# Optimization experiments

Hardware: AMD Instinct MI355X
Metric: run time of the kernel (lower is better)

## Reference

```python
import jax, jax.numpy as jnp
import numpy as np

V, FC = 6890, 13776
N, H, W, K = 2, 336, 336, 28
SIGMA, GAMMA, EPS = 1e-4, 1e-4, 1e-10
ZNEAR, ZFAR = 1.0, 100.0
SHININESS = 64.0
BG = jnp.array([1.0, 1.0, 1.0], jnp.float32)


def setup_inputs() -> dict:
    key = jax.random.key(0)
    ks = jax.random.split(key, 10)
    verts = jax.random.normal(ks[0], (V, 3), jnp.float32)
    vert_colors = jax.random.uniform(ks[1], (V, 3), jnp.float32)
    faces = jax.random.randint(ks[2], (FC, 3), 0, V)
    # shift so ~1/FC entries are -1 (background), as in PyTorch3D Fragments
    pix_to_face = jax.random.randint(ks[3], (N, H, W, K), 0, FC + 1) - 1
    u = jax.random.uniform(ks[4], (N, H, W, K, 3), jnp.float32) + 1e-3
    bary_coords = u / u.sum(-1, keepdims=True)
    dists = jax.random.normal(ks[5], (N, H, W, K), jnp.float32) * 1e-4
    zbuf = jnp.sort(jax.random.uniform(ks[6], (N, H, W, K), jnp.float32) * 10.0 + 2.0, axis=-1)
    light_location = jnp.array([0.0, 0.0, 10.0], jnp.float32)
    ambient_color = jnp.full((3,), 0.5, jnp.float32)
    diffuse_color = jnp.full((3,), 0.3, jnp.float32)
    specular_color = jnp.full((3,), 0.2, jnp.float32)
    camera_position = jnp.array([0.0, 0.0, 2.7], jnp.float32)
    return dict(verts=verts, vert_colors=vert_colors, faces=faces,
                pix_to_face=pix_to_face, bary_coords=bary_coords, dists=dists,
                zbuf=zbuf, light_location=light_location,
                ambient_color=ambient_color, diffuse_color=diffuse_color,
                specular_color=specular_color, camera_position=camera_position)


def _normalize(x, eps=1e-6):
    return x / jnp.maximum(jnp.linalg.norm(x, axis=-1, keepdims=True), eps)


def reference(verts, vert_colors, faces, pix_to_face, bary_coords, dists, zbuf,
              light_location, ambient_color, diffuse_color, specular_color,
              camera_position):
    # ---- per-vertex normals (area-weighted face normals scatter-added) ----
    v0, v1, v2 = verts[faces[:, 0]], verts[faces[:, 1]], verts[faces[:, 2]]
    fn = jnp.cross(v1 - v0, v2 - v0)                       # [F,3]
    fn_rep = jnp.repeat(fn[:, None, :], 3, axis=1).reshape(-1, 3)
    vnorm = jax.ops.segment_sum(fn_rep, faces.reshape(-1), num_segments=verts.shape[0])
    vnorm = _normalize(vnorm)                              # [V,3]

    # ---- gather face attributes per fragment & barycentric interpolation ----
    mask = pix_to_face >= 0                                # [N,H,W,K]
    idx = jnp.maximum(pix_to_face, 0)
    f = faces[idx]                                         # [N,H,W,K,3]
    pix_pos = jnp.einsum('nhwkc,nhwkcd->nhwkd', bary_coords, verts[f])
    pix_nrm = _normalize(jnp.einsum('nhwkc,nhwkcd->nhwkd', bary_coords, vnorm[f]))
    texels = jnp.einsum('nhwkc,nhwkcd->nhwkd', bary_coords, vert_colors[f])

    # ---- Phong shading (point light) ----
    l = _normalize(light_location - pix_pos)               # [N,H,W,K,3]
    ndotl = jnp.maximum(jnp.sum(pix_nrm * l, axis=-1), 0.0)
    diffuse = diffuse_color * ndotl[..., None]
    view = _normalize(camera_position - pix_pos)
    reflect = -l + 2.0 * jnp.sum(l * pix_nrm, axis=-1, keepdims=True) * pix_nrm
    cos_a = jnp.maximum(jnp.sum(reflect * view, axis=-1), 0.0)
    specular = specular_color * (cos_a ** SHININESS)[..., None]
    colors = (ambient_color + diffuse) * texels + specular  # [N,H,W,K,3]

    # ---- softmax_rgb_blend ----
    prob = jax.nn.sigmoid(-dists / SIGMA) * mask            # [N,H,W,K]
    z_inv = jnp.where(mask, (ZFAR - zbuf) / (ZFAR - ZNEAR), 0.0)
    z_inv_max = jnp.maximum(z_inv.max(axis=-1, keepdims=True), EPS)
    w_num = prob * jnp.exp((z_inv - z_inv_max) / GAMMA)     # [N,H,W,K]
    delta = jnp.exp((EPS - z_inv_max) / GAMMA)              # [N,H,W,1]
    denom = w_num.sum(axis=-1, keepdims=True) + delta       # [N,H,W,1]
    rgb = (jnp.einsum('nhwk,nhwkd->nhwd', w_num, colors) + delta * BG) / denom
    alpha = 1.0 - jnp.prod(1.0 - prob, axis=-1)             # [N,H,W]
    images = jnp.concatenate([rgb, alpha[..., None]], axis=-1)  # [N,H,W,4]
    return images, zbuf
```

## Files before the change

kernel.cpp:

```cpp
#include <hip/hip_runtime.h>
#include <hip/hip_fp16.h>
#include <math.h>

#define V_   6890
#define FC_  13776
#define N_   2
#define H_   336
#define W_   336
#define K_   28
#define NPIX (N_*H_*W_)

#define SIGMA_INV 1.0e4f
#define GAMMA_INV 1.0e4f
#define EPS_      1e-10f
#define ZFAR_     100.0f
#define ZSCALE    (1.0f/99.0f)
#define LOG2E     1.442695041f
#define SKIP_EXPONENT 25.0f

typedef float f32x4 __attribute__((ext_vector_type(4)));

static __device__ __forceinline__ float fexp(float x)  { return __builtin_amdgcn_exp2f(x * LOG2E); }
static __device__ __forceinline__ float frcp(float x)  { return __builtin_amdgcn_rcpf(x); }
static __device__ __forceinline__ float frsq(float x)  { return __builtin_amdgcn_rsqf(x); }

#define FD_OFFSET 82944

union FaceRec { uint4 q[4]; float f[16]; __half h[32]; unsigned char b[64]; };

__global__ __launch_bounds__(256)
void face_normals(const float* __restrict__ verts,
                  const int*   __restrict__ faces,
                  float* __restrict__ vnAcc) {
    int i = blockIdx.x * blockDim.x + threadIdx.x;
    if (i >= FC_) return;
    int f0 = faces[i*3+0], f1 = faces[i*3+1], f2 = faces[i*3+2];
    float p0x = verts[f0*3+0], p0y = verts[f0*3+1], p0z = verts[f0*3+2];
    float p1x = verts[f1*3+0], p1y = verts[f1*3+1], p1z = verts[f1*3+2];
    float p2x = verts[f2*3+0], p2y = verts[f2*3+1], p2z = verts[f2*3+2];
    float e1x = p1x-p0x, e1y = p1y-p0y, e1z = p1z-p0z;
    float e2x = p2x-p0x, e2y = p2y-p0y, e2z = p2z-p0z;
    float fnx = e1y*e2z - e1z*e2y;
    float fny = e1z*e2x - e1x*e2z;
    float fnz = e1x*e2y - e1y*e2x;
    atomicAdd(&vnAcc[f0*3+0], fnx); atomicAdd(&vnAcc[f0*3+1], fny); atomicAdd(&vnAcc[f0*3+2], fnz);
    atomicAdd(&vnAcc[f1*3+0], fnx); atomicAdd(&vnAcc[f1*3+1], fny); atomicAdd(&vnAcc[f1*3+2], fnz);
    atomicAdd(&vnAcc[f2*3+0], fnx); atomicAdd(&vnAcc[f2*3+1], fny); atomicAdd(&vnAcc[f2*3+2], fnz);
}

__global__ __launch_bounds__(256)
void face_pack(const int*   __restrict__ faces,
               const float* __restrict__ verts,
               const float* __restrict__ vcol,
               const float* __restrict__ vn,
               uint4* __restrict__ fd) {
    int i = blockIdx.x * blockDim.x + threadIdx.x;
    if (i >= FC_) return;
    FaceRec R;
    #pragma unroll
    for (int v = 0; v < 3; ++v) {
        int fv = faces[i*3+v];
        R.f[v*3+0] = verts[fv*3+0];
        R.f[v*3+1] = verts[fv*3+1];
        R.f[v*3+2] = verts[fv*3+2];
        float nx = vn[fv*3+0], ny = vn[fv*3+1], nz = vn[fv*3+2];
        float inv = frsq(fmaxf(nx*nx + ny*ny + nz*nz, 1e-12f));
        R.h[18+v*3+0] = __float2half(nx*inv);
        R.h[18+v*3+1] = __float2half(ny*inv);
        R.h[18+v*3+2] = __float2half(nz*inv);
        R.b[54+v*3+0] = (unsigned char)lrintf(vcol[fv*3+0]*255.0f);
        R.b[54+v*3+1] = (unsigned char)lrintf(vcol[fv*3+1]*255.0f);
        R.b[54+v*3+2] = (unsigned char)lrintf(vcol[fv*3+2]*255.0f);
    }
    R.b[63] = 0;
    uint4* o = fd + (size_t)i * 4;
    o[0] = R.q[0]; o[1] = R.q[1]; o[2] = R.q[2]; o[3] = R.q[3];
}

__global__ __launch_bounds__(256)
void pixel_kernel(const int*   __restrict__ ptf,
                  const float* __restrict__ bary,
                  const float* __restrict__ dists,
                  const float* __restrict__ zbuf,
                  const uint4* __restrict__ fd,
                  const float* __restrict__ light,
                  const float* __restrict__ amb,
                  const float* __restrict__ dif,
                  const float* __restrict__ spec,
                  const float* __restrict__ cam,
                  float* __restrict__ out) {
    int tid = blockIdx.x * blockDim.x + threadIdx.x;
    int pix = tid >> 3;
    int j   = tid & 7;

    float lx = light[0], ly = light[1], lz = light[2];
    float cx = cam[0],   cy = cam[1],   cz = cam[2];
    float a0 = amb[0],  a1 = amb[1],  a2 = amb[2];
    float f0 = dif[0],  f1 = dif[1],  f2 = dif[2];
    float s0 = spec[0], s1 = spec[1], s2 = spec[2];

    float wsum = 0.0f, sr = 0.0f, sg = 0.0f, sb = 0.0f;
    float om = 1.0f;
    float mloc = 0.0f;

    int   pfs[4]  = {-1,-1,-1,-1};
    float zi[4]   = {0,0,0,0};
    float prob[4] = {0,0,0,0};
    bool lane_act = (j < 7);
    size_t sbase = (size_t)pix * K_ + (size_t)j * 4;

    if (lane_act) {
        int4   pf4 = *(const int4*)  (ptf   + sbase);
        float4 d4  = *(const float4*)(dists + sbase);
        float4 z4  = *(const float4*)(zbuf  + sbase);

        f32x4 znt = { z4.x, z4.y, z4.z, z4.w };
        __builtin_nontemporal_store(znt, (f32x4*)(out + (size_t)NPIX*4 + sbase));

        pfs[0]=pf4.x; pfs[1]=pf4.y; pfs[2]=pf4.z; pfs[3]=pf4.w;
        float ds_[4] = {d4.x, d4.y, d4.z, d4.w};
        float zs_[4] = {z4.x, z4.y, z4.z, z4.w};

        #pragma unroll
        for (int s = 0; s < 4; ++s) {
            zi[s] = (ZFAR_ - zs_[s]) * ZSCALE;
            bool a = (pfs[s] >= 0);
            float pr = frcp(1.0f + fexp(ds_[s] * SIGMA_INV));
            prob[s] = a ? pr : 0.0f;
            if (a) mloc = fmaxf(mloc, zi[s]);
            om *= (1.0f - prob[s]);
        }
    }

    float m = mloc;
    m = fmaxf(m, __shfl_xor(m, 1));
    m = fmaxf(m, __shfl_xor(m, 2));
    m = fmaxf(m, __shfl_xor(m, 4));
    m = fmaxf(m, EPS_);

    #pragma unroll
    for (int s = 0; s < 4; ++s) {
        float ex = (zi[s] - m) * GAMMA_INV;
        bool keep = (pfs[s] >= 0) && (ex >= -SKIP_EXPONENT);
        if (keep) {
            size_t smp = sbase + (size_t)s;
            float3 bv = *(const float3*)(bary + smp*3);
            float w0 = bv.x, w1 = bv.y, w2 = bv.z;

            FaceRec F;
            const uint4* g = fd + (size_t)pfs[s] * 4;
            F.q[0] = g[0]; F.q[1] = g[1]; F.q[2] = g[2]; F.q[3] = g[3];

            float px = w0*F.f[0] + w1*F.f[3] + w2*F.f[6];
            float py = w0*F.f[1] + w1*F.f[4] + w2*F.f[7];
            float pz = w0*F.f[2] + w1*F.f[5] + w2*F.f[8];
            float nux = w0*__half2float(F.h[18]) + w1*__half2float(F.h[21]) + w2*__half2float(F.h[24]);
            float nuy = w0*__half2float(F.h[19]) + w1*__half2float(F.h[22]) + w2*__half2float(F.h[25]);
            float nuz = w0*__half2float(F.h[20]) + w1*__half2float(F.h[23]) + w2*__half2float(F.h[26]);
            const float s255 = 1.0f/255.0f;
            float tr = (w0*(float)F.b[54] + w1*(float)F.b[57] + w2*(float)F.b[60]) * s255;
            float tg = (w0*(float)F.b[55] + w1*(float)F.b[58] + w2*(float)F.b[61]) * s255;
            float tb = (w0*(float)F.b[56] + w1*(float)F.b[59] + w2*(float)F.b[62]) * s255;

            float ninv = frsq(fmaxf(nux*nux + nuy*nuy + nuz*nuz, 1e-12f));
            float nx = nux*ninv, ny = nuy*ninv, nz = nuz*ninv;

            float lvx = lx - px, lvy = ly - py, lvz = lz - pz;
            float linv = frsq(fmaxf(lvx*lvx + lvy*lvy + lvz*lvz, 1e-12f));
            lvx *= linv; lvy *= linv; lvz *= linv;
            float ldn = lvx*nx + lvy*ny + lvz*nz;
            float ndotl = fmaxf(ldn, 0.0f);

            float vvx = cx - px, vvy = cy - py, vvz = cz - pz;
            float vinv = frsq(fmaxf(vvx*vvx + vvy*vvy + vvz*vvz, 1e-12f));
            vvx *= vinv; vvy *= vinv; vvz *= vinv;

            float rx = 2.0f*ldn*nx - lvx;
            float ry = 2.0f*ldn*ny - lvy;
            float rz = 2.0f*ldn*nz - lvz;
            float ca = fmaxf(rx*vvx + ry*vvy + rz*vvz, 0.0f);
            float p64 = ca*ca; p64 *= p64; p64 *= p64; p64 *= p64; p64 *= p64; p64 *= p64;

            float cr = (a0 + f0*ndotl)*tr + s0*p64;
            float cg = (a1 + f1*ndotl)*tg + s1*p64;
            float cb = (a2 + f2*ndotl)*tb + s2*p64;

            float w = prob[s] * fexp(ex);
            wsum += w; sr += w*cr; sg += w*cg; sb += w*cb;
        }
    }

    #pragma unroll
    for (int o = 4; o; o >>= 1) {
        wsum += __shfl_xor(wsum, o);
        sr   += __shfl_xor(sr,   o);
        sg   += __shfl_xor(sg,   o);
        sb   += __shfl_xor(sb,   o);
        om   *= __shfl_xor(om,   o);
    }

    if (j == 0) {
        float deltaw = fexp((EPS_ - m) * GAMMA_INV);
        float inv = frcp(wsum + deltaw);
        float4 img;
        img.x = (sr + deltaw) * inv;
        img.y = (sg + deltaw) * inv;
        img.z = (sb + deltaw) * inv;
        img.w = 1.0f - om;
        ((float4*)out)[pix] = img;
    }
}

extern "C" void kernel_launch(void* const* d_in, const int* in_sizes, int n_in,
                              void* d_out, int out_size, void* d_ws, size_t ws_size,
                              hipStream_t stream) {
    const float* verts = (const float*)d_in[0];
    const float* vcol  = (const float*)d_in[1];
    const int*   faces = (const int*)d_in[2];
    const int*   ptf   = (const int*)d_in[3];
    const float* bary  = (const float*)d_in[4];
    const float* dists = (const float*)d_in[5];
    const float* zbuf  = (const float*)d_in[6];
    const float* light = (const float*)d_in[7];
    const float* amb   = (const float*)d_in[8];
    const float* dif   = (const float*)d_in[9];
    const float* spec  = (const float*)d_in[10];
    const float* cam   = (const float*)d_in[11];
    float* out = (float*)d_out;

    float* vnAcc = (float*)d_ws;
    uint4* fdat  = (uint4*)((char*)d_ws + FD_OFFSET);

    (void)hipMemsetAsync(vnAcc, 0, (size_t)V_ * 3 * sizeof(float), stream);
    face_normals<<<(FC_ + 255)/256, 256, 0, stream>>>(verts, faces, vnAcc);
    face_pack<<<(FC_ + 255)/256, 256, 0, stream>>>(faces, verts, vcol, vnAcc, fdat);

    int blocks = (NPIX * 8) / 256;
    pixel_kernel<<<blocks, 256, 0, stream>>>(
        ptf, bary, dists, zbuf, fdat,
        light, amb, dif, spec, cam, out);
}
```

Measured before the change: 216.8 us.

## Fuse memset, normals, pack and pixel kernels into one cooperative persistent kernel

Replaces the memset plus three kernel launches with a single cooperative kernel that uses grid-wide syncs between the zeroing, face-normal accumulation, face packing and pixel shading phases. The pixel phase becomes a grid-stride loop over a persistent grid sized from the occupancy query. The aim is to remove launch gaps and per-kernel tail effects. In exchange it adds three grid barriers, the cooperative launch overhead, and the occupancy query on the host every call. The small prologue phases also run on a limited grid, and register pressure from the fused code may lower occupancy.

```diff
diff --git a/kernel.cpp b/kernel.cpp
--- a/kernel.cpp
+++ b/kernel.cpp
@@ -1,6 +1,9 @@
 #include <hip/hip_runtime.h>
+#include <hip/hip_cooperative_groups.h>
 #include <hip/hip_fp16.h>
 #include <math.h>
+
+namespace cg = cooperative_groups;
 
 #define V_   6890
 #define FC_  13776
@@ -28,70 +31,67 @@
 
 union FaceRec { uint4 q[4]; float f[16]; __half h[32]; unsigned char b[64]; };
 
-__global__ __launch_bounds__(256)
-void face_normals(const float* __restrict__ verts,
-                  const int*   __restrict__ faces,
-                  float* __restrict__ vnAcc) {
-    int i = blockIdx.x * blockDim.x + threadIdx.x;
-    if (i >= FC_) return;
-    int f0 = faces[i*3+0], f1 = faces[i*3+1], f2 = faces[i*3+2];
-    float p0x = verts[f0*3+0], p0y = verts[f0*3+1], p0z = verts[f0*3+2];
-    float p1x = verts[f1*3+0], p1y = verts[f1*3+1], p1z = verts[f1*3+2];
-    float p2x = verts[f2*3+0], p2y = verts[f2*3+1], p2z = verts[f2*3+2];
-    float e1x = p1x-p0x, e1y = p1y-p0y, e1z = p1z-p0z;
-    float e2x = p2x-p0x, e2y = p2y-p0y, e2z = p2z-p0z;
-    float fnx = e1y*e2z - e1z*e2y;
-    float fny = e1z*e2x - e1x*e2z;
-    float fnz = e1x*e2y - e1y*e2x;
-    atomicAdd(&vnAcc[f0*3+0], fnx); atomicAdd(&vnAcc[f0*3+1], fny); atomicAdd(&vnAcc[f0*3+2], fnz);
-    atomicAdd(&vnAcc[f1*3+0], fnx); atomicAdd(&vnAcc[f1*3+1], fny); atomicAdd(&vnAcc[f1*3+2], fnz);
-    atomicAdd(&vnAcc[f2*3+0], fnx); atomicAdd(&vnAcc[f2*3+1], fny); atomicAdd(&vnAcc[f2*3+2], fnz);
-}
-
-__global__ __launch_bounds__(256)
-void face_pack(const int*   __restrict__ faces,
-               const float* __restrict__ verts,
-               const float* __restrict__ vcol,
-               const float* __restrict__ vn,
-               uint4* __restrict__ fd) {
-    int i = blockIdx.x * blockDim.x + threadIdx.x;
-    if (i >= FC_) return;
-    FaceRec R;
-    #pragma unroll
-    for (int v = 0; v < 3; ++v) {
-        int fv = faces[i*3+v];
-        R.f[v*3+0] = verts[fv*3+0];
-        R.f[v*3+1] = verts[fv*3+1];
-        R.f[v*3+2] = verts[fv*3+2];
-        float nx = vn[fv*3+0], ny = vn[fv*3+1], nz = vn[fv*3+2];
-        float inv = frsq(fmaxf(nx*nx + ny*ny + nz*nz, 1e-12f));
-        R.h[18+v*3+0] = __float2half(nx*inv);
-        R.h[18+v*3+1] = __float2half(ny*inv);
-        R.h[18+v*3+2] = __float2half(nz*inv);
-        R.b[54+v*3+0] = (unsigned char)lrintf(vcol[fv*3+0]*255.0f);
-        R.b[54+v*3+1] = (unsigned char)lrintf(vcol[fv*3+1]*255.0f);
-        R.b[54+v*3+2] = (unsigned char)lrintf(vcol[fv*3+2]*255.0f);
+__global__ __launch_bounds__(256, 8)
+void mega_kernel(const float* __restrict__ verts,
+                 const float* __restrict__ vcol,
+                 const int*   __restrict__ faces,
+                 const int*   __restrict__ ptf,
+                 const float* __restrict__ bary,
+                 const float* __restrict__ dists,
+                 const float* __restrict__ zbuf,
+                 const float* __restrict__ light,
+                 const float* __restrict__ amb,
+                 const float* __restrict__ dif,
+                 const float* __restrict__ spec,
+                 const float* __restrict__ cam,
+                 float* __restrict__ vnAcc,
+                 uint4* __restrict__ fd,
+                 float* __restrict__ out) {
+    cg::grid_group grid = cg::this_grid();
+    int tid0   = blockIdx.x * blockDim.x + threadIdx.x;
+    int stride = gridDim.x * blockDim.x;
+
+    for (int i = tid0; i < 3*V_; i += stride) vnAcc[i] = 0.0f;
+    grid.sync();
+
+    for (int i = tid0; i < FC_; i += stride) {
+        int f0 = faces[i*3+0], f1 = faces[i*3+1], f2 = faces[i*3+2];
+        float p0x = verts[f0*3+0], p0y = verts[f0*3+1], p0z = verts[f0*3+2];
+        float p1x = verts[f1*3+0], p1y = verts[f1*3+1], p1z = verts[f1*3+2];
+        float p2x = verts[f2*3+0], p2y = verts[f2*3+1], p2z = verts[f2*3+2];
+        float e1x = p1x-p0x, e1y = p1y-p0y, e1z = p1z-p0z;
+        float e2x = p2x-p0x, e2y = p2y-p0y, e2z = p2z-p0z;
+        float fnx = e1y*e2z - e1z*e2y;
+        float fny = e1z*e2x - e1x*e2z;
+        float fnz = e1x*e2y - e1y*e2x;
+        atomicAdd(&vnAcc[f0*3+0], fnx); atomicAdd(&vnAcc[f0*3+1], fny); atomicAdd(&vnAcc[f0*3+2], fnz);
+        atomicAdd(&vnAcc[f1*3+0], fnx); atomicAdd(&vnAcc[f1*3+1], fny); atomicAdd(&vnAcc[f1*3+2], fnz);
+        atomicAdd(&vnAcc[f2*3+0], fnx); atomicAdd(&vnAcc[f2*3+1], fny); atomicAdd(&vnAcc[f2*3+2], fnz);
     }
-    R.b[63] = 0;
-    uint4* o = fd + (size_t)i * 4;
-    o[0] = R.q[0]; o[1] = R.q[1]; o[2] = R.q[2]; o[3] = R.q[3];
-}
-
-__global__ __launch_bounds__(256)
-void pixel_kernel(const int*   __restrict__ ptf,
-                  const float* __restrict__ bary,
-                  const float* __restrict__ dists,
-                  const float* __restrict__ zbuf,
-                  const uint4* __restrict__ fd,
-                  const float* __restrict__ light,
-                  const float* __restrict__ amb,
-                  const float* __restrict__ dif,
-                  const float* __restrict__ spec,
-                  const float* __restrict__ cam,
-                  float* __restrict__ out) {
-    int tid = blockIdx.x * blockDim.x + threadIdx.x;
-    int pix = tid >> 3;
-    int j   = tid & 7;
+    grid.sync();
+
+    for (int i = tid0; i < FC_; i += stride) {
+        FaceRec R;
+        #pragma unroll
+        for (int v = 0; v < 3; ++v) {
+            int fv = faces[i*3+v];
+            R.f[v*3+0] = verts[fv*3+0];
+            R.f[v*3+1] = verts[fv*3+1];
+            R.f[v*3+2] = verts[fv*3+2];
+            float nx = vnAcc[fv*3+0], ny = vnAcc[fv*3+1], nz = vnAcc[fv*3+2];
+            float inv = frsq(fmaxf(nx*nx + ny*ny + nz*nz, 1e-12f));
+            R.h[18+v*3+0] = __float2half(nx*inv);
+            R.h[18+v*3+1] = __float2half(ny*inv);
+            R.h[18+v*3+2] = __float2half(nz*inv);
+            R.b[54+v*3+0] = (unsigned char)lrintf(vcol[fv*3+0]*255.0f);
+            R.b[54+v*3+1] = (unsigned char)lrintf(vcol[fv*3+1]*255.0f);
+            R.b[54+v*3+2] = (unsigned char)lrintf(vcol[fv*3+2]*255.0f);
+        }
+        R.b[63] = 0;
+        uint4* o = fd + (size_t)i * 4;
+        o[0] = R.q[0]; o[1] = R.q[1]; o[2] = R.q[2]; o[3] = R.q[3];
+    }
+    grid.sync();
 
     float lx = light[0], ly = light[1], lz = light[2];
     float cx = cam[0],   cy = cam[1],   cz = cam[2];
@@ -99,115 +99,121 @@
     float f0 = dif[0],  f1 = dif[1],  f2 = dif[2];
     float s0 = spec[0], s1 = spec[1], s2 = spec[2];
 
-    float wsum = 0.0f, sr = 0.0f, sg = 0.0f, sb = 0.0f;
-    float om = 1.0f;
-    float mloc = 0.0f;
-
-    int   pfs[4]  = {-1,-1,-1,-1};
-    float zi[4]   = {0,0,0,0};
-    float prob[4] = {0,0,0,0};
-    bool lane_act = (j < 7);
-    size_t sbase = (size_t)pix * K_ + (size_t)j * 4;
-
-    if (lane_act) {
-        int4   pf4 = *(const int4*)  (ptf   + sbase);
-        float4 d4  = *(const float4*)(dists + sbase);
-        float4 z4  = *(const float4*)(zbuf  + sbase);
-
-        f32x4 znt = { z4.x, z4.y, z4.z, z4.w };
-        __builtin_nontemporal_store(znt, (f32x4*)(out + (size_t)NPIX*4 + sbase));
-
-        pfs[0]=pf4.x; pfs[1]=pf4.y; pfs[2]=pf4.z; pfs[3]=pf4.w;
-        float ds_[4] = {d4.x, d4.y, d4.z, d4.w};
-        float zs_[4] = {z4.x, z4.y, z4.z, z4.w};
+    const int T = NPIX * 8;
+    for (int t = tid0; t < T; t += stride) {
+        int pix = t >> 3;
+        int j   = t & 7;
+
+        float wsum = 0.0f, sr = 0.0f, sg = 0.0f, sb = 0.0f;
+        float om = 1.0f;
+        float mloc = 0.0f;
+
+        int   pfs[4]  = {-1,-1,-1,-1};
+        float zi[4]   = {0,0,0,0};
+        float prob[4] = {0,0,0,0};
+        bool lane_act = (j < 7);
+        size_t sbase = (size_t)pix * K_ + (size_t)j * 4;
+
+        if (lane_act) {
+            int4   pf4 = *(const int4*)  (ptf   + sbase);
+            float4 d4  = *(const float4*)(dists + sbase);
+            float4 z4  = *(const float4*)(zbuf  + sbase);
+
+            f32x4 znt = { z4.x, z4.y, z4.z, z4.w };
+            __builtin_nontemporal_store(znt, (f32x4*)(out + (size_t)NPIX*4 + sbase));
+
+            pfs[0]=pf4.x; pfs[1]=pf4.y; pfs[2]=pf4.z; pfs[3]=pf4.w;
+            float ds_[4] = {d4.x, d4.y, d4.z, d4.w};
+            float zs_[4] = {z4.x, z4.y, z4.z, z4.w};
+
+            #pragma unroll
+            for (int s = 0; s < 4; ++s) {
+                zi[s] = (ZFAR_ - zs_[s]) * ZSCALE;
+                bool a = (pfs[s] >= 0);
+                float pr = frcp(1.0f + fexp(ds_[s] * SIGMA_INV));
+                prob[s] = a ? pr : 0.0f;
+                if (a) mloc = fmaxf(mloc, zi[s]);
+                om *= (1.0f - prob[s]);
+            }
+        }
+
+        float m = mloc;
+        m = fmaxf(m, __shfl_xor(m, 1));
+        m = fmaxf(m, __shfl_xor(m, 2));
+        m = fmaxf(m, __shfl_xor(m, 4));
+        m = fmaxf(m, EPS_);
 
         #pragma unroll
         for (int s = 0; s < 4; ++s) {
-            zi[s] = (ZFAR_ - zs_[s]) * ZSCALE;
-            bool a = (pfs[s] >= 0);
-            float pr = frcp(1.0f + fexp(ds_[s] * SIGMA_INV));
-            prob[s] = a ? pr : 0.0f;
-            if (a) mloc = fmaxf(mloc, zi[s]);
-            om *= (1.0f - prob[s]);
-        }
-    }
-
-    float m = mloc;
-    m = fmaxf(m, __shfl_xor(m, 1));
-    m = fmaxf(m, __shfl_xor(m, 2));
-    m = fmaxf(m, __shfl_xor(m, 4));
-    m = fmaxf(m, EPS_);
-
-    #pragma unroll
-    for (int s = 0; s < 4; ++s) {
-        float ex = (zi[s] - m) * GAMMA_INV;
-        bool keep = (pfs[s] >= 0) && (ex >= -SKIP_EXPONENT);
-        if (keep) {
-            size_t smp = sbase + (size_t)s;
-            float3 bv = *(const float3*)(bary + smp*3);
-            float w0 = bv.x, w1 = bv.y, w2 = bv.z;
-
-            FaceRec F;
-            const uint4* g = fd + (size_t)pfs[s] * 4;
-            F.q[0] = g[0]; F.q[1] = g[1]; F.q[2] = g[2]; F.q[3] = g[3];
-
-            float px = w0*F.f[0] + w1*F.f[3] + w2*F.f[6];
-            float py = w0*F.f[1] + w1*F.f[4] + w2*F.f[7];
-            float pz = w0*F.f[2] + w1*F.f[5] + w2*F.f[8];
-            float nux = w0*__half2float(F.h[18]) + w1*__half2float(F.h[21]) + w2*__half2float(F.h[24]);
-            float nuy = w0*__half2float(F.h[19]) + w1*__half2float(F.h[22]) + w2*__half2float(F.h[25]);
-            float nuz = w0*__half2float(F.h[20]) + w1*__half2float(F.h[23]) + w2*__half2float(F.h[26]);
-            const float s255 = 1.0f/255.0f;
-            float tr = (w0*(float)F.b[54] + w1*(float)F.b[57] + w2*(float)F.b[60]) * s255;
-            float tg = (w0*(float)F.b[55] + w1*(float)F.b[58] + w2*(float)F.b[61]) * s255;
-            float tb = (w0*(float)F.b[56] + w1*(float)F.b[59] + w2*(float)F.b[62]) * s255;
-
-            float ninv = frsq(fmaxf(nux*nux + nuy*nuy + nuz*nuz, 1e-12f));
-            float nx = nux*ninv, ny = nuy*ninv, nz = nuz*ninv;
-
-            float lvx = lx - px, lvy = ly - py, lvz = lz - pz;
-            float linv = frsq(fmaxf(lvx*lvx + lvy*lvy + lvz*lvz, 1e-12f));
-            lvx *= linv; lvy *= linv; lvz *= linv;
-            float ldn = lvx*nx + lvy*ny + lvz*nz;
-            float ndotl = fmaxf(ldn, 0.0f);
-
-            float vvx = cx - px, vvy = cy - py, vvz = cz - pz;
-            float vinv = frsq(fmaxf(vvx*vvx + vvy*vvy + vvz*vvz, 1e-12f));
-            vvx *= vinv; vvy *= vinv; vvz *= vinv;
-
-            float rx = 2.0f*ldn*nx - lvx;
-            float ry = 2.0f*ldn*ny - lvy;
-            float rz = 2.0f*ldn*nz - lvz;
-            float ca = fmaxf(rx*vvx + ry*vvy + rz*vvz, 0.0f);
-            float p64 = ca*ca; p64 *= p64; p64 *= p64; p64 *= p64; p64 *= p64; p64 *= p64;
-
-            float cr = (a0 + f0*ndotl)*tr + s0*p64;
-            float cg = (a1 + f1*ndotl)*tg + s1*p64;
-            float cb = (a2 + f2*ndotl)*tb + s2*p64;
-
-            float w = prob[s] * fexp(ex);
-            wsum += w; sr += w*cr; sg += w*cg; sb += w*cb;
-        }
-    }
-
-    #pragma unroll
-    for (int o = 4; o; o >>= 1) {
-        wsum += __shfl_xor(wsum, o);
-        sr   += __shfl_xor(sr,   o);
-        sg   += __shfl_xor(sg,   o);
-        sb   += __shfl_xor(sb,   o);
-        om   *= __shfl_xor(om,   o);
-    }
-
-    if (j == 0) {
-        float deltaw = fexp((EPS_ - m) * GAMMA_INV);
-        float inv = frcp(wsum + deltaw);
-        float4 img;
-        img.x = (sr + deltaw) * inv;
-        img.y = (sg + deltaw) * inv;
-        img.z = (sb + deltaw) * inv;
-        img.w = 1.0f - om;
-        ((float4*)out)[pix] = img;
+            float ex = (zi[s] - m) * GAMMA_INV;
+            bool keep = (pfs[s] >= 0) && (ex >= -SKIP_EXPONENT);
+            if (keep) {
+                size_t smp = sbase + (size_t)s;
+                float3 bv = *(const float3*)(bary + smp*3);
+                float w0 = bv.x, w1 = bv.y, w2 = bv.z;
+
+                FaceRec F;
+                const uint4* g = fd + (size_t)pfs[s] * 4;
+                F.q[0] = g[0]; F.q[1] = g[1]; F.q[2] = g[2]; F.q[3] = g[3];
+
+                float px = w0*F.f[0] + w1*F.f[3] + w2*F.f[6];
+                float py = w0*F.f[1] + w1*F.f[4] + w2*F.f[7];
+                float pz = w0*F.f[2] + w1*F.f[5] + w2*F.f[8];
+                float nux = w0*__half2float(F.h[18]) + w1*__half2float(F.h[21]) + w2*__half2float(F.h[24]);
+                float nuy = w0*__half2float(F.h[19]) + w1*__half2float(F.h[22]) + w2*__half2float(F.h[25]);
+                float nuz = w0*__half2float(F.h[20]) + w1*__half2float(F.h[23]) + w2*__half2float(F.h[26]);
+                const float s255 = 1.0f/255.0f;
+                float tr = (w0*(float)F.b[54] + w1*(float)F.b[57] + w2*(float)F.b[60]) * s255;
+                float tg = (w0*(float)F.b[55] + w1*(float)F.b[58] + w2*(float)F.b[61]) * s255;
+                float tb = (w0*(float)F.b[56] + w1*(float)F.b[59] + w2*(float)F.b[62]) * s255;
+
+                float ninv = frsq(fmaxf(nux*nux + nuy*nuy + nuz*nuz, 1e-12f));
+                float nx = nux*ninv, ny = nuy*ninv, nz = nuz*ninv;
+
+                float lvx = lx - px, lvy = ly - py, lvz = lz - pz;
+                float linv = frsq(fmaxf(lvx*lvx + lvy*lvy + lvz*lvz, 1e-12f));
+                lvx *= linv; lvy *= linv; lvz *= linv;
+                float ldn = lvx*nx + lvy*ny + lvz*nz;
+                float ndotl = fmaxf(ldn, 0.0f);
+
+                float vvx = cx - px, vvy = cy - py, vvz = cz - pz;
+                float vinv = frsq(fmaxf(vvx*vvx + vvy*vvy + vvz*vvz, 1e-12f));
+                vvx *= vinv; vvy *= vinv; vvz *= vinv;
+
+                float rx = 2.0f*ldn*nx - lvx;
+                float ry = 2.0f*ldn*ny - lvy;
+                float rz = 2.0f*ldn*nz - lvz;
+                float ca = fmaxf(rx*vvx + ry*vvy + rz*vvz, 0.0f);
+                float p64 = ca*ca; p64 *= p64; p64 *= p64; p64 *= p64; p64 *= p64; p64 *= p64;
+
+                float cr = (a0 + f0*ndotl)*tr + s0*p64;
+                float cg = (a1 + f1*ndotl)*tg + s1*p64;
+                float cb = (a2 + f2*ndotl)*tb + s2*p64;
+
+                float w = prob[s] * fexp(ex);
+                wsum += w; sr += w*cr; sg += w*cg; sb += w*cb;
+            }
+        }
+
+        #pragma unroll
+        for (int o = 4; o; o >>= 1) {
+            wsum += __shfl_xor(wsum, o);
+            sr   += __shfl_xor(sr,   o);
+            sg   += __shfl_xor(sg,   o);
+            sb   += __shfl_xor(sb,   o);
+            om   *= __shfl_xor(om,   o);
+        }
+
+        if (j == 0) {
+            float deltaw = fexp((EPS_ - m) * GAMMA_INV);
+            float inv = frcp(wsum + deltaw);
+            float4 img;
+            img.x = (sr + deltaw) * inv;
+            img.y = (sg + deltaw) * inv;
+            img.z = (sb + deltaw) * inv;
+            img.w = 1.0f - om;
+            ((float4*)out)[pix] = img;
+        }
     }
 }
 
@@ -231,12 +237,18 @@
     float* vnAcc = (float*)d_ws;
     uint4* fdat  = (uint4*)((char*)d_ws + FD_OFFSET);
 
-    (void)hipMemsetAsync(vnAcc, 0, (size_t)V_ * 3 * sizeof(float), stream);
-    face_normals<<<(FC_ + 255)/256, 256, 0, stream>>>(verts, faces, vnAcc);
-    face_pack<<<(FC_ + 255)/256, 256, 0, stream>>>(faces, verts, vcol, vnAcc, fdat);
-
-    int blocks = (NPIX * 8) / 256;
-    pixel_kernel<<<blocks, 256, 0, stream>>>(
-        ptf, bary, dists, zbuf, fdat,
-        light, amb, dif, spec, cam, out);
+    int maxBlocksPerCU = 0;
+    (void)hipOccupancyMaxActiveBlocksPerMultiprocessor(&maxBlocksPerCU,
+            (const void*)mega_kernel, 256, 0);
+    if (maxBlocksPerCU < 1) maxBlocksPerCU = 1;
+    int blocks = maxBlocksPerCU * 256;
+    if (blocks > 2048) blocks = 2048;
+
+    void* args[] = { (void*)&verts, (void*)&vcol, (void*)&faces, (void*)&ptf,
+                     (void*)&bary, (void*)&dists, (void*)&zbuf, (void*)&light,
+                     (void*)&amb, (void*)&dif, (void*)&spec, (void*)&cam,
+                     (void*)&vnAcc, (void*)&fdat, (void*)&out };
+    (void)hipLaunchCooperativeKernel((const void*)mega_kernel,
+                                     dim3(blocks), dim3(256),
+                                     args, 0, stream);
 }
```

Measured after the change: 500.8 us. 131% more time.

## Fuse memset, face normals and face packing into one single-block LDS kernel

Applied to the files above, without the earlier changes.

Replaces the memset plus two face-preprocessing kernels with one 1024-thread single-block kernel. Vertex normals are accumulated with LDS atomics in shared memory (about 83 KB) instead of global atomics. This removes two launches, the memset and the global atomic traffic. The cost is that only one CU does all the face work serially across about 14 iterations per thread, which may lengthen this stage.

```diff
diff --git a/kernel.cpp b/kernel.cpp
--- a/kernel.cpp
+++ b/kernel.cpp
@@ -24,57 +24,56 @@
 static __device__ __forceinline__ float frcp(float x)  { return __builtin_amdgcn_rcpf(x); }
 static __device__ __forceinline__ float frsq(float x)  { return __builtin_amdgcn_rsqf(x); }
 
-#define FD_OFFSET 82944
-
 union FaceRec { uint4 q[4]; float f[16]; __half h[32]; unsigned char b[64]; };
 
-__global__ __launch_bounds__(256)
-void face_normals(const float* __restrict__ verts,
-                  const int*   __restrict__ faces,
-                  float* __restrict__ vnAcc) {
-    int i = blockIdx.x * blockDim.x + threadIdx.x;
-    if (i >= FC_) return;
-    int f0 = faces[i*3+0], f1 = faces[i*3+1], f2 = faces[i*3+2];
-    float p0x = verts[f0*3+0], p0y = verts[f0*3+1], p0z = verts[f0*3+2];
-    float p1x = verts[f1*3+0], p1y = verts[f1*3+1], p1z = verts[f1*3+2];
-    float p2x = verts[f2*3+0], p2y = verts[f2*3+1], p2z = verts[f2*3+2];
-    float e1x = p1x-p0x, e1y = p1y-p0y, e1z = p1z-p0z;
-    float e2x = p2x-p0x, e2y = p2y-p0y, e2z = p2z-p0z;
-    float fnx = e1y*e2z - e1z*e2y;
-    float fny = e1z*e2x - e1x*e2z;
-    float fnz = e1x*e2y - e1y*e2x;
-    atomicAdd(&vnAcc[f0*3+0], fnx); atomicAdd(&vnAcc[f0*3+1], fny); atomicAdd(&vnAcc[f0*3+2], fnz);
-    atomicAdd(&vnAcc[f1*3+0], fnx); atomicAdd(&vnAcc[f1*3+1], fny); atomicAdd(&vnAcc[f1*3+2], fnz);
-    atomicAdd(&vnAcc[f2*3+0], fnx); atomicAdd(&vnAcc[f2*3+1], fny); atomicAdd(&vnAcc[f2*3+2], fnz);
-}
-
-__global__ __launch_bounds__(256)
-void face_pack(const int*   __restrict__ faces,
-               const float* __restrict__ verts,
-               const float* __restrict__ vcol,
-               const float* __restrict__ vn,
-               uint4* __restrict__ fd) {
-    int i = blockIdx.x * blockDim.x + threadIdx.x;
-    if (i >= FC_) return;
-    FaceRec R;
-    #pragma unroll
-    for (int v = 0; v < 3; ++v) {
-        int fv = faces[i*3+v];
-        R.f[v*3+0] = verts[fv*3+0];
-        R.f[v*3+1] = verts[fv*3+1];
-        R.f[v*3+2] = verts[fv*3+2];
-        float nx = vn[fv*3+0], ny = vn[fv*3+1], nz = vn[fv*3+2];
-        float inv = frsq(fmaxf(nx*nx + ny*ny + nz*nz, 1e-12f));
-        R.h[18+v*3+0] = __float2half(nx*inv);
-        R.h[18+v*3+1] = __float2half(ny*inv);
-        R.h[18+v*3+2] = __float2half(nz*inv);
-        R.b[54+v*3+0] = (unsigned char)lrintf(vcol[fv*3+0]*255.0f);
-        R.b[54+v*3+1] = (unsigned char)lrintf(vcol[fv*3+1]*255.0f);
-        R.b[54+v*3+2] = (unsigned char)lrintf(vcol[fv*3+2]*255.0f);
-    }
-    R.b[63] = 0;
-    uint4* o = fd + (size_t)i * 4;
-    o[0] = R.q[0]; o[1] = R.q[1]; o[2] = R.q[2]; o[3] = R.q[3];
+__global__ __launch_bounds__(1024)
+void face_kernel(const float* __restrict__ verts,
+                 const float* __restrict__ vcol,
+                 const int*   __restrict__ faces,
+                 uint4* __restrict__ fd) {
+    __shared__ float vn[3*V_];
+    int tid = threadIdx.x;
+
+    for (int i = tid; i < 3*V_; i += 1024) vn[i] = 0.0f;
+    __syncthreads();
+
+    for (int i = tid; i < FC_; i += 1024) {
+        int f0 = faces[i*3+0], f1 = faces[i*3+1], f2 = faces[i*3+2];
+        float p0x = verts[f0*3+0], p0y = verts[f0*3+1], p0z = verts[f0*3+2];
+        float p1x = verts[f1*3+0], p1y = verts[f1*3+1], p1z = verts[f1*3+2];
+        float p2x = verts[f2*3+0], p2y = verts[f2*3+1], p2z = verts[f2*3+2];
+        float e1x = p1x-p0x, e1y = p1y-p0y, e1z = p1z-p0z;
+        float e2x = p2x-p0x, e2y = p2y-p0y, e2z = p2z-p0z;
+        float fnx = e1y*e2z - e1z*e2y;
+        float fny = e1z*e2x - e1x*e2z;
+        float fnz = e1x*e2y - e1y*e2x;
+        atomicAdd(&vn[f0*3+0], fnx); atomicAdd(&vn[f0*3+1], fny); atomicAdd(&vn[f0*3+2], fnz);
+        atomicAdd(&vn[f1*3+0], fnx); atomicAdd(&vn[f1*3+1], fny); atomicAdd(&vn[f1*3+2], fnz);
+        atomicAdd(&vn[f2*3+0], fnx); atomicAdd(&vn[f2*3+1], fny); atomicAdd(&vn[f2*3+2], fnz);
+    }
+    __syncthreads();
+
+    for (int i = tid; i < FC_; i += 1024) {
+        FaceRec R;
+        #pragma unroll
+        for (int v = 0; v < 3; ++v) {
+            int fv = faces[i*3+v];
+            R.f[v*3+0] = verts[fv*3+0];
+            R.f[v*3+1] = verts[fv*3+1];
+            R.f[v*3+2] = verts[fv*3+2];
+            float nx = vn[fv*3+0], ny = vn[fv*3+1], nz = vn[fv*3+2];
+            float inv = frsq(fmaxf(nx*nx + ny*ny + nz*nz, 1e-12f));
+            R.h[18+v*3+0] = __float2half(nx*inv);
+            R.h[18+v*3+1] = __float2half(ny*inv);
+            R.h[18+v*3+2] = __float2half(nz*inv);
+            R.b[54+v*3+0] = (unsigned char)lrintf(vcol[fv*3+0]*255.0f);
+            R.b[54+v*3+1] = (unsigned char)lrintf(vcol[fv*3+1]*255.0f);
+            R.b[54+v*3+2] = (unsigned char)lrintf(vcol[fv*3+2]*255.0f);
+        }
+        R.b[63] = 0;
+        uint4* o = fd + (size_t)i * 4;
+        o[0] = R.q[0]; o[1] = R.q[1]; o[2] = R.q[2]; o[3] = R.q[3];
+    }
 }
 
 __global__ __launch_bounds__(256)
@@ -228,12 +227,9 @@
     const float* cam   = (const float*)d_in[11];
     float* out = (float*)d_out;
 
-    float* vnAcc = (float*)d_ws;
-    uint4* fdat  = (uint4*)((char*)d_ws + FD_OFFSET);
-
-    (void)hipMemsetAsync(vnAcc, 0, (size_t)V_ * 3 * sizeof(float), stream);
-    face_normals<<<(FC_ + 255)/256, 256, 0, stream>>>(verts, faces, vnAcc);
-    face_pack<<<(FC_ + 255)/256, 256, 0, stream>>>(faces, verts, vcol, vnAcc, fdat);
+    uint4* fdat = (uint4*)d_ws;
+
+    face_kernel<<<1, 1024, 0, stream>>>(verts, vcol, faces, fdat);
 
     int blocks = (NPIX * 8) / 256;
     pixel_kernel<<<blocks, 256, 0, stream>>>(
```

Result: slower. 446.9 us (+106.1%).

## Process each pixel with one thread using sorted-depth max instead of 8-lane split

Applied to the files above, without the earlier changes.

Switches the pixel kernel from 8 lanes per pixel with shuffle reductions to one thread per pixel. Each thread loads all 28 samples' face ids, dists and zbuf into registers. Instead of a separate reduction pass for the depth max, it takes the first active sample's inverse depth as the max, relying on zbuf being sorted ascending, and shades in a single pass. This removes the cross-lane shuffles and the two-phase structure. In exchange it launches 8x fewer threads, makes each lane's loads strided and poorly coalesced, and raises register pressure.

```diff
diff --git a/kernel.cpp b/kernel.cpp
--- a/kernel.cpp
+++ b/kernel.cpp
@@ -89,9 +89,22 @@
                   const float* __restrict__ spec,
                   const float* __restrict__ cam,
                   float* __restrict__ out) {
-    int tid = blockIdx.x * blockDim.x + threadIdx.x;
-    int pix = tid >> 3;
-    int j   = tid & 7;
+    int pix = blockIdx.x * blockDim.x + threadIdx.x;
+    size_t base = (size_t)pix * K_;
+
+    int4   pf4[7];
+    float4 d4[7], z4[7];
+    #pragma unroll
+    for (int c = 0; c < 7; ++c) {
+        pf4[c] = *(const int4*)  (ptf   + base + c*4);
+        d4[c]  = *(const float4*)(dists + base + c*4);
+        z4[c]  = *(const float4*)(zbuf  + base + c*4);
+    }
+    #pragma unroll
+    for (int c = 0; c < 7; ++c) {
+        f32x4 znt = { z4[c].x, z4[c].y, z4[c].z, z4[c].w };
+        __builtin_nontemporal_store(znt, (f32x4*)(out + (size_t)NPIX*4 + base + c*4));
+    }
 
     float lx = light[0], ly = light[1], lz = light[2];
     float cx = cam[0],   cy = cam[1],   cz = cam[2];
@@ -101,114 +114,81 @@
 
     float wsum = 0.0f, sr = 0.0f, sg = 0.0f, sb = 0.0f;
     float om = 1.0f;
-    float mloc = 0.0f;
-
-    int   pfs[4]  = {-1,-1,-1,-1};
-    float zi[4]   = {0,0,0,0};
-    float prob[4] = {0,0,0,0};
-    bool lane_act = (j < 7);
-    size_t sbase = (size_t)pix * K_ + (size_t)j * 4;
-
-    if (lane_act) {
-        int4   pf4 = *(const int4*)  (ptf   + sbase);
-        float4 d4  = *(const float4*)(dists + sbase);
-        float4 z4  = *(const float4*)(zbuf  + sbase);
-
-        f32x4 znt = { z4.x, z4.y, z4.z, z4.w };
-        __builtin_nontemporal_store(znt, (f32x4*)(out + (size_t)NPIX*4 + sbase));
-
-        pfs[0]=pf4.x; pfs[1]=pf4.y; pfs[2]=pf4.z; pfs[3]=pf4.w;
-        float ds_[4] = {d4.x, d4.y, d4.z, d4.w};
-        float zs_[4] = {z4.x, z4.y, z4.z, z4.w};
-
+    float m  = -3.0e38f;
+
+    #pragma unroll
+    for (int c = 0; c < 7; ++c) {
+        int   pfs[4] = {pf4[c].x, pf4[c].y, pf4[c].z, pf4[c].w};
+        float ds_[4] = {d4[c].x, d4[c].y, d4[c].z, d4[c].w};
+        float zs_[4] = {z4[c].x, z4[c].y, z4[c].z, z4[c].w};
         #pragma unroll
         for (int s = 0; s < 4; ++s) {
-            zi[s] = (ZFAR_ - zs_[s]) * ZSCALE;
-            bool a = (pfs[s] >= 0);
+            bool active = (pfs[s] >= 0);
             float pr = frcp(1.0f + fexp(ds_[s] * SIGMA_INV));
-            prob[s] = a ? pr : 0.0f;
-            if (a) mloc = fmaxf(mloc, zi[s]);
-            om *= (1.0f - prob[s]);
+            if (active) om *= (1.0f - pr);
+            float zi = (ZFAR_ - zs_[s]) * ZSCALE;
+            if (active) {
+                if (m == -3.0e38f) m = zi;
+                float ex = (zi - m) * GAMMA_INV;
+                if (ex >= -SKIP_EXPONENT) {
+                    size_t smp = base + (size_t)(c*4 + s);
+                    float3 bv = *(const float3*)(bary + smp*3);
+                    float w0 = bv.x, w1 = bv.y, w2 = bv.z;
+
+                    FaceRec F;
+                    const uint4* g = fd + (size_t)pfs[s] * 4;
+                    F.q[0] = g[0]; F.q[1] = g[1]; F.q[2] = g[2]; F.q[3] = g[3];
+
+                    float px = w0*F.f[0] + w1*F.f[3] + w2*F.f[6];
+                    float py = w0*F.f[1] + w1*F.f[4] + w2*F.f[7];
+                    float pz = w0*F.f[2] + w1*F.f[5] + w2*F.f[8];
+                    float nux = w0*__half2float(F.h[18]) + w1*__half2float(F.h[21]) + w2*__half2float(F.h[24]);
+                    float nuy = w0*__half2float(F.h[19]) + w1*__half2float(F.h[22]) + w2*__half2float(F.h[25]);
+                    float nuz = w0*__half2float(F.h[20]) + w1*__half2float(F.h[23]) + w2*__half2float(F.h[26]);
+                    const float s255 = 1.0f/255.0f;
+                    float tr = (w0*(float)F.b[54] + w1*(float)F.b[57] + w2*(float)F.b[60]) * s255;
+                    float tg = (w0*(float)F.b[55] + w1*(float)F.b[58] + w2*(float)F.b[61]) * s255;
+                    float tb = (w0*(float)F.b[56] + w1*(float)F.b[59] + w2*(float)F.b[62]) * s255;
+
+                    float ninv = frsq(fmaxf(nux*nux + nuy*nuy + nuz*nuz, 1e-12f));
+                    float nx = nux*ninv, ny = nuy*ninv, nz = nuz*ninv;
+
+                    float lvx = lx - px, lvy = ly - py, lvz = lz - pz;
+                    float linv = frsq(fmaxf(lvx*lvx + lvy*lvy + lvz*lvz, 1e-12f));
+                    lvx *= linv; lvy *= linv; lvz *= linv;
+                    float ldn = lvx*nx + lvy*ny + lvz*nz;
+                    float ndotl = fmaxf(ldn, 0.0f);
+
+                    float vvx = cx - px, vvy = cy - py, vvz = cz - pz;
+                    float vinv = frsq(fmaxf(vvx*vvx + vvy*vvy + vvz*vvz, 1e-12f));
+                    vvx *= vinv; vvy *= vinv; vvz *= vinv;
+
+                    float rx = 2.0f*ldn*nx - lvx;
+                    float ry = 2.0f*ldn*ny - lvy;
+                    float rz = 2.0f*ldn*nz - lvz;
+                    float ca = fmaxf(rx*vvx + ry*vvy + rz*vvz, 0.0f);
+                    float p64 = ca*ca; p64 *= p64; p64 *= p64; p64 *= p64; p64 *= p64; p64 *= p64;
+
+                    float cr = (a0 + f0*ndotl)*tr + s0*p64;
+                    float cg = (a1 + f1*ndotl)*tg + s1*p64;
+                    float cb = (a2 + f2*ndotl)*tb + s2*p64;
+
+                    float w = pr * fexp(ex);
+                    wsum += w; sr += w*cr; sg += w*cg; sb += w*cb;
+                }
+            }
         }
     }
 
-    float m = mloc;
-    m = fmaxf(m, __shfl_xor(m, 1));
-    m = fmaxf(m, __shfl_xor(m, 2));
-    m = fmaxf(m, __shfl_xor(m, 4));
-    m = fmaxf(m, EPS_);
-
-    #pragma unroll
-    for (int s = 0; s < 4; ++s) {
-        float ex = (zi[s] - m) * GAMMA_INV;
-        bool keep = (pfs[s] >= 0) && (ex >= -SKIP_EXPONENT);
-        if (keep) {
-            size_t smp = sbase + (size_t)s;
-            float3 bv = *(const float3*)(bary + smp*3);
-            float w0 = bv.x, w1 = bv.y, w2 = bv.z;
-
-            FaceRec F;
-            const uint4* g = fd + (size_t)pfs[s] * 4;
-            F.q[0] = g[0]; F.q[1] = g[1]; F.q[2] = g[2]; F.q[3] = g[3];
-
-            float px = w0*F.f[0] + w1*F.f[3] + w2*F.f[6];
-            float py = w0*F.f[1] + w1*F.f[4] + w2*F.f[7];
-            float pz = w0*F.f[2] + w1*F.f[5] + w2*F.f[8];
-            float nux = w0*__half2float(F.h[18]) + w1*__half2float(F.h[21]) + w2*__half2float(F.h[24]);
-            float nuy = w0*__half2float(F.h[19]) + w1*__half2float(F.h[22]) + w2*__half2float(F.h[25]);
-            float nuz = w0*__half2float(F.h[20]) + w1*__half2float(F.h[23]) + w2*__half2float(F.h[26]);
-            const float s255 = 1.0f/255.0f;
-            float tr = (w0*(float)F.b[54] + w1*(float)F.b[57] + w2*(float)F.b[60]) * s255;
-            float tg = (w0*(float)F.b[55] + w1*(float)F.b[58] + w2*(float)F.b[61]) * s255;
-            float tb = (w0*(float)F.b[56] + w1*(float)F.b[59] + w2*(float)F.b[62]) * s255;
-
-            float ninv = frsq(fmaxf(nux*nux + nuy*nuy + nuz*nuz, 1e-12f));
-            float nx = nux*ninv, ny = nuy*ninv, nz = nuz*ninv;
-
-            float lvx = lx - px, lvy = ly - py, lvz = lz - pz;
-            float linv = frsq(fmaxf(lvx*lvx + lvy*lvy + lvz*lvz, 1e-12f));
-            lvx *= linv; lvy *= linv; lvz *= linv;
-            float ldn = lvx*nx + lvy*ny + lvz*nz;
-            float ndotl = fmaxf(ldn, 0.0f);
-
-            float vvx = cx - px, vvy = cy - py, vvz = cz - pz;
-            float vinv = frsq(fmaxf(vvx*vvx + vvy*vvy + vvz*vvz, 1e-12f));
-            vvx *= vinv; vvy *= vinv; vvz *= vinv;
-
-            float rx = 2.0f*ldn*nx - lvx;
-            float ry = 2.0f*ldn*ny - lvy;
-            float rz = 2.0f*ldn*nz - lvz;
-            float ca = fmaxf(rx*vvx + ry*vvy + rz*vvz, 0.0f);
-            float p64 = ca*ca; p64 *= p64; p64 *= p64; p64 *= p64; p64 *= p64; p64 *= p64;
-
-            float cr = (a0 + f0*ndotl)*tr + s0*p64;
-            float cg = (a1 + f1*ndotl)*tg + s1*p64;
-            float cb = (a2 + f2*ndotl)*tb + s2*p64;
-
-            float w = prob[s] * fexp(ex);
-            wsum += w; sr += w*cr; sg += w*cg; sb += w*cb;
-        }
-    }
-
-    #pragma unroll
-    for (int o = 4; o; o >>= 1) {
-        wsum += __shfl_xor(wsum, o);
-        sr   += __shfl_xor(sr,   o);
-        sg   += __shfl_xor(sg,   o);
-        sb   += __shfl_xor(sb,   o);
-        om   *= __shfl_xor(om,   o);
-    }
-
-    if (j == 0) {
-        float deltaw = fexp((EPS_ - m) * GAMMA_INV);
-        float inv = frcp(wsum + deltaw);
-        float4 img;
-        img.x = (sr + deltaw) * inv;
-        img.y = (sg + deltaw) * inv;
-        img.z = (sb + deltaw) * inv;
-        img.w = 1.0f - om;
-        ((float4*)out)[pix] = img;
-    }
+    float mm = fmaxf(m, EPS_);
+    float deltaw = fexp((EPS_ - mm) * GAMMA_INV);
+    float inv = frcp(wsum + deltaw);
+    float4 img;
+    img.x = (sr + deltaw) * inv;
+    img.y = (sg + deltaw) * inv;
+    img.z = (sb + deltaw) * inv;
+    img.w = 1.0f - om;
+    ((float4*)out)[pix] = img;
 }
 
 extern "C" void kernel_launch(void* const* d_in, const int* in_sizes, int n_in,
@@ -235,7 +215,7 @@
     face_normals<<<(FC_ + 255)/256, 256, 0, stream>>>(verts, faces, vnAcc);
     face_pack<<<(FC_ + 255)/256, 256, 0, stream>>>(faces, verts, vcol, vnAcc, fdat);
 
-    int blocks = (NPIX * 8) / 256;
+    int blocks = NPIX / 256;
     pixel_kernel<<<blocks, 256, 0, stream>>>(
         ptf, bary, dists, zbuf, fdat,
         light, amb, dif, spec, cam, out);
```

Result: slower. 252.7 us (+16.6%).
